# Kernel optimization log

Measured on AMD Instinct MI355X. Metric: run time of the kernel, lower is better.

## Reference

```python
import jax, jax.numpy as jnp
import numpy as np

N_NODES = 50000
N_EDGES = 1600000
DIM = 128
BN_EPS = 1e-5


def setup_inputs() -> dict:
    key = jax.random.key(0)
    k1, k2, k3 = jax.random.split(key, 3)
    x = jax.random.normal(k1, (N_NODES, DIM), dtype=jnp.float32)
    edge_index = jax.random.randint(k2, (2, N_EDGES), 0, N_NODES, dtype=jnp.int32)
    W = jax.random.normal(k3, (DIM, DIM), dtype=jnp.float32) / np.float32(np.sqrt(DIM))
    b = jnp.zeros((DIM,), dtype=jnp.float32)
    gamma = jnp.ones((DIM,), dtype=jnp.float32)
    beta = jnp.zeros((DIM,), dtype=jnp.float32)
    return {"x": x, "W": W, "b": b, "gamma": gamma, "beta": beta, "edge_index": edge_index}


def reference(x, W, b, gamma, beta, edge_index):
    """ResGCNBlock: relu(BN(GCNConv(x, edge_index))) + x (PyG GCNConv semantics)."""
    n = x.shape[0]
    # GCNConv: linear transform first
    h = x @ W  # [N, D]
    # add self-loops
    loop = jnp.arange(n, dtype=edge_index.dtype)
    src = jnp.concatenate([edge_index[0], loop])  # [E+N]
    dst = jnp.concatenate([edge_index[1], loop])
    # symmetric normalization: deg over targets (edge weight = 1)
    deg = jax.ops.segment_sum(jnp.ones_like(dst, dtype=h.dtype), dst, num_segments=n)
    dinv = jax.lax.rsqrt(jnp.maximum(deg, 1e-12))  # deg >= 1 due to self-loops
    norm = dinv[src] * dinv[dst]  # [E+N]
    # gather -> scale -> scatter-add
    agg = jax.ops.segment_sum(h[src] * norm[:, None], dst, num_segments=n) + b  # [N, D]
    # BatchNorm1d (training mode: batch stats over node dim, biased variance)
    mean = jnp.mean(agg, axis=0)
    var = jnp.mean(jnp.square(agg - mean), axis=0)
    y = gamma * (agg - mean) * jax.lax.rsqrt(var + BN_EPS) + beta
    return jax.nn.relu(y) + x
```

## Files before the change

### kernel.cpp

```cpp
#include <hip/hip_runtime.h>

#define DIM 128

__device__ __forceinline__ float bf_to_f(unsigned short v) {
    return __uint_as_float(((unsigned int)v) << 16);
}
__device__ __forceinline__ unsigned short f_to_bf(float f) {
    unsigned int u = __float_as_uint(f);
    u += 0x7FFFu + ((u >> 16) & 1u);
    return (unsigned short)(u >> 16);
}
__device__ __forceinline__ bool probe_bf16(const void* gamma) {
    return *reinterpret_cast<const unsigned int*>(gamma) != 0x3F800000u;
}

__global__ __launch_bounds__(256) void k_deg(const int* __restrict__ ei,
                                             int* __restrict__ deg, int E) {
    int t = blockIdx.x * 256 + threadIdx.x;
    if (t < E) atomicAdd(&deg[ei[E + t]], 1);
}
__global__ __launch_bounds__(256) void k_dinv(const int* __restrict__ deg,
                                              float* __restrict__ dinv, int N) {
    int t = blockIdx.x * 256 + threadIdx.x;
    if (t < N) dinv[t] = rsqrtf((float)deg[t] + 1.0f);
}

#define EPB 4096

__global__ __launch_bounds__(256) void k_cbhist(const int* __restrict__ ei,
                                                int* __restrict__ thist, int E) {
    __shared__ int hist[256];
    const int t = threadIdx.x;
    const int e0 = blockIdx.x * EPB;
    hist[t] = 0;
    __syncthreads();
    #pragma unroll
    for (int u = 0; u < 16; u++) {
        const int i = e0 + t + u * 256;
        if (i < E) atomicAdd(&hist[((unsigned int)ei[E + i]) >> 8], 1);
    }
    __syncthreads();
    if (hist[t] > 0) atomicAdd(&thist[t], hist[t]);
}

__global__ __launch_bounds__(256) void k_bscan2(const int* __restrict__ thist,
                                                int* __restrict__ bbase,
                                                int* __restrict__ ccur) {
    __shared__ int sh[256];
    const int t = threadIdx.x;
    const int v = thist[t];
    sh[t] = v;
    __syncthreads();
    for (int off = 1; off < 256; off <<= 1) {
        int u = (t >= off) ? sh[t - off] : 0;
        __syncthreads();
        sh[t] += u;
        __syncthreads();
    }
    bbase[t + 1] = sh[t];
    ccur[t] = sh[t] - v;
    if (t == 0) bbase[0] = 0;
}

__global__ __launch_bounds__(256) void k_partition(
    const int* __restrict__ ei, int* __restrict__ ccur,
    unsigned int* __restrict__ epart, int E)
{
    __shared__ int hist[256];
    __shared__ int scan_tmp[256];
    __shared__ int lbase[256];
    __shared__ int lcur[256];
    __shared__ int gbase[256];
    __shared__ unsigned int sorted[EPB];
    const int t = threadIdx.x;
    const int e0 = blockIdx.x * EPB;
    const int ecount = min(EPB, E - e0);
    hist[t] = 0; lcur[t] = 0;
    __syncthreads();

    unsigned int ent[16];
    #pragma unroll
    for (int u = 0; u < 16; u++) {
        const int i = e0 + t + u * 256;
        if (i < E) {
            const unsigned int src = (unsigned int)ei[i];
            const unsigned int dst = (unsigned int)ei[E + i];
            const unsigned int cb = dst >> 8;
            ent[u] = src | ((dst & 255u) << 16) | (cb << 24);
            atomicAdd(&hist[cb], 1);
        } else ent[u] = 0xFFFFFFFFu;
    }
    __syncthreads();
    scan_tmp[t] = hist[t];
    __syncthreads();
    for (int off = 1; off < 256; off <<= 1) {
        int v = (t >= off) ? scan_tmp[t - off] : 0;
        __syncthreads();
        scan_tmp[t] += v;
        __syncthreads();
    }
    lbase[t] = scan_tmp[t] - hist[t];
    __syncthreads();
    #pragma unroll
    for (int u = 0; u < 16; u++) {
        if (ent[u] != 0xFFFFFFFFu) {
            const int cb = (int)(ent[u] >> 24);
            const int pos = lbase[cb] + atomicAdd(&lcur[cb], 1);
            sorted[pos] = ent[u];
        }
    }
    if (hist[t] > 0) gbase[t] = atomicAdd(&ccur[t], hist[t]);
    __syncthreads();
    for (int s = t; s < ecount; s += 256) {
        const unsigned int e = sorted[s];
        const int cb = (int)(e >> 24);
        epart[gbase[cb] + (s - lbase[cb])] = e;
    }
}

__global__ __launch_bounds__(256) void k_fine2(
    const unsigned int* __restrict__ epart, const int* __restrict__ bbase,
    int* __restrict__ rowptr, float* __restrict__ dinv,
    int* __restrict__ esrc, int N)
{
    __shared__ int ldeg[256];
    __shared__ int sh[256];
    __shared__ int lex[256];
    __shared__ int lcur[256];
    const int cb = blockIdx.x;
    const int t = threadIdx.x;
    const int beg = bbase[cb];
    const int end = bbase[cb + 1];
    ldeg[t] = 0; lcur[t] = 0;
    __syncthreads();

    for (int i = beg + t; i < end; i += 256)
        atomicAdd(&ldeg[(epart[i] >> 16) & 255u], 1);
    __syncthreads();
    sh[t] = ldeg[t];
    __syncthreads();
    for (int off = 1; off < 256; off <<= 1) {
        int v = (t >= off) ? sh[t - off] : 0;
        __syncthreads();
        sh[t] += v;
        __syncthreads();
    }
    lex[t] = sh[t] - ldeg[t];
    __syncthreads();

    const int node = (cb << 8) + t;
    if (node < N) {
        rowptr[node] = beg + lex[t];
        dinv[node] = rsqrtf((float)ldeg[t] + 1.0f);
        if (node == N - 1) rowptr[N] = beg + lex[t] + ldeg[t];
    }

    for (int i = beg + t; i < end; i += 256) {
        const unsigned int e = epart[i];
        const int d = (int)((e >> 16) & 255u);
        const int pos = beg + lex[d] + atomicAdd(&lcur[d], 1);
        esrc[pos] = (int)(e & 0xFFFFu);
    }
}

__global__ __launch_bounds__(256, 4) void k_gemm(
    const void* __restrict__ xv, const void* __restrict__ Wv,
    const void* __restrict__ bv, const void* __restrict__ probe,
    const float* __restrict__ dinv, unsigned short* __restrict__ h,
    float* __restrict__ agg, int N, int wr_seed)
{
    const bool isbf = probe_bf16(probe);
    __shared__ __align__(16) unsigned short Wsb[DIM * 64];
    __shared__ __align__(16) float xs[64 * 132];
    const int t  = threadIdx.x;
    const int ch = blockIdx.x & 1;
    const int r0 = (blockIdx.x >> 1) * 64;

    if (isbf) {
        const unsigned short* W = (const unsigned short*)Wv;
        for (int s = 4 * t; s < DIM * 64; s += 1024) {
            const int k = s >> 6, c = s & 63;
            *reinterpret_cast<ushort4*>(Wsb + s) =
                *reinterpret_cast<const ushort4*>(W + k * DIM + ch * 64 + c);
        }
    } else {
        const float* W = (const float*)Wv;
        for (int s = 4 * t; s < DIM * 64; s += 1024) {
            const int k = s >> 6, c = s & 63;
            const float4 w = *reinterpret_cast<const float4*>(W + k * DIM + ch * 64 + c);
            ushort4 p;
            p.x = f_to_bf(w.x); p.y = f_to_bf(w.y);
            p.z = f_to_bf(w.z); p.w = f_to_bf(w.w);
            *reinterpret_cast<ushort4*>(Wsb + s) = p;
        }
    }
    for (int idx = 4 * t; idx < 64 * DIM; idx += 1024) {
        const int row = idx >> 7, k = idx & 127;
        const int r = r0 + row;
        float4 v = make_float4(0.f, 0.f, 0.f, 0.f);
        if (r < N) {
            if (isbf) {
                ushort4 u = *reinterpret_cast<const ushort4*>(
                    (const unsigned short*)xv + (size_t)r * DIM + k);
                v.x = bf_to_f(u.x); v.y = bf_to_f(u.y);
                v.z = bf_to_f(u.z); v.w = bf_to_f(u.w);
            } else {
                v = *reinterpret_cast<const float4*>((const float*)xv + (size_t)r * DIM + k);
            }
        }
        *reinterpret_cast<float4*>(xs + row * 132 + k) = v;
    }
    __syncthreads();

    const int c4 = t & 15;
    const int rg = t >> 4;
    float acc[4][4] = {{0,0,0,0},{0,0,0,0},{0,0,0,0},{0,0,0,0}};
    #pragma unroll 2
    for (int k = 0; k < DIM; k += 4) {
        const ushort4 wu0 = *reinterpret_cast<const ushort4*>(Wsb + (k + 0) * 64 + 4 * c4);
        const ushort4 wu1 = *reinterpret_cast<const ushort4*>(Wsb + (k + 1) * 64 + 4 * c4);
        const ushort4 wu2 = *reinterpret_cast<const ushort4*>(Wsb + (k + 2) * 64 + 4 * c4);
        const ushort4 wu3 = *reinterpret_cast<const ushort4*>(Wsb + (k + 3) * 64 + 4 * c4);
        float w[4][4];
        w[0][0] = bf_to_f(wu0.x); w[0][1] = bf_to_f(wu0.y);
        w[0][2] = bf_to_f(wu0.z); w[0][3] = bf_to_f(wu0.w);
        w[1][0] = bf_to_f(wu1.x); w[1][1] = bf_to_f(wu1.y);
        w[1][2] = bf_to_f(wu1.z); w[1][3] = bf_to_f(wu1.w);
        w[2][0] = bf_to_f(wu2.x); w[2][1] = bf_to_f(wu2.y);
        w[2][2] = bf_to_f(wu2.z); w[2][3] = bf_to_f(wu2.w);
        w[3][0] = bf_to_f(wu3.x); w[3][1] = bf_to_f(wu3.y);
        w[3][2] = bf_to_f(wu3.z); w[3][3] = bf_to_f(wu3.w);
        #pragma unroll
        for (int j = 0; j < 4; j++) {
            const float4 xk = *reinterpret_cast<const float4*>(&xs[(rg + 16 * j) * 132 + k]);
            #pragma unroll
            for (int cc = 0; cc < 4; cc++) {
                acc[j][cc] = fmaf(xk.x, w[0][cc], acc[j][cc]);
                acc[j][cc] = fmaf(xk.y, w[1][cc], acc[j][cc]);
                acc[j][cc] = fmaf(xk.z, w[2][cc], acc[j][cc]);
                acc[j][cc] = fmaf(xk.w, w[3][cc], acc[j][cc]);
            }
        }
    }
    const int gc = ch * 64 + 4 * c4;
    #pragma unroll
    for (int j = 0; j < 4; j++) {
        const int r = r0 + rg + 16 * j;
        if (r < N) {
            const float di = dinv[r];
            ushort4 hp;
            hp.x = f_to_bf(acc[j][0] * di); hp.y = f_to_bf(acc[j][1] * di);
            hp.z = f_to_bf(acc[j][2] * di); hp.w = f_to_bf(acc[j][3] * di);
            *reinterpret_cast<ushort4*>(h + (size_t)r * DIM + gc) = hp;
            if (wr_seed) {
                float4 bc;
                if (isbf) {
                    const unsigned short* bb = (const unsigned short*)bv;
                    bc.x = bf_to_f(bb[gc]); bc.y = bf_to_f(bb[gc + 1]);
                    bc.z = bf_to_f(bb[gc + 2]); bc.w = bf_to_f(bb[gc + 3]);
                } else {
                    bc = *reinterpret_cast<const float4*>((const float*)bv + gc);
                }
                const float di2 = di * di;
                float4 av;
                av.x = fmaf(acc[j][0], di2, bc.x);
                av.y = fmaf(acc[j][1], di2, bc.y);
                av.z = fmaf(acc[j][2], di2, bc.z);
                av.w = fmaf(acc[j][3], di2, bc.w);
                *reinterpret_cast<float4*>(agg + (size_t)r * DIM + gc) = av;
            }
        }
    }
}

__device__ __forceinline__ float2 load_h2(const unsigned short* __restrict__ h,
                                          int src, int lane) {
    const unsigned int u = *reinterpret_cast<const unsigned int*>(
        h + (size_t)src * DIM + 2 * lane);
    return make_float2(bf_to_f((unsigned short)(u & 0xFFFFu)),
                       bf_to_f((unsigned short)(u >> 16)));
}

__global__ __launch_bounds__(256) void k_agg(
    const int* __restrict__ rowptr, const int* __restrict__ esrc,
    const unsigned short* __restrict__ h, const float* __restrict__ dinv,
    const void* __restrict__ bv, const void* __restrict__ probe,
    float* __restrict__ agg, int N)
{
    const int lane = threadIdx.x & 63;
    const int node = __builtin_amdgcn_readfirstlane(
        (int)((blockIdx.x * 256 + threadIdx.x) >> 6));
    if (node >= N) return;

    const int beg = rowptr[node];
    const int end = rowptr[node + 1];
    const float didst = dinv[node];
    const unsigned int* __restrict__ hu = (const unsigned int*)h;

    float a0 = 0.f, a1 = 0.f;

    {
        const unsigned int v = hu[(size_t)node * 64 + lane];
        a0 += __uint_as_float(v << 16);
        a1 += __uint_as_float(v & 0xFFFF0000u);
    }

    const int lm = end - 1;
    for (int j = beg; j < end; j += 16) {
        const int myidx = esrc[min(j + (lane & 15), lm)];
        unsigned int uv[16];
        #pragma unroll
        for (int u = 0; u < 16; u++) {
            const int s = __builtin_amdgcn_readlane(myidx, u);
            uv[u] = hu[(size_t)s * 64 + lane];
        }
        #pragma unroll
        for (int u = 0; u < 16; u++) {
            const float sel = (j + u < end) ? 1.0f : 0.0f;
            a0 = fmaf(__uint_as_float(uv[u] << 16), sel, a0);
            a1 = fmaf(__uint_as_float(uv[u] & 0xFFFF0000u), sel, a1);
        }
    }

    const int gc = 2 * lane;
    float b0, b1;
    if (probe_bf16(probe)) {
        const unsigned int bb = *reinterpret_cast<const unsigned int*>(
            (const unsigned short*)bv + gc);
        b0 = bf_to_f((unsigned short)(bb & 0xFFFFu));
        b1 = bf_to_f((unsigned short)(bb >> 16));
    } else {
        const float2 bf = *reinterpret_cast<const float2*>((const float*)bv + gc);
        b0 = bf.x; b1 = bf.y;
    }
    float2 o;
    o.x = fmaf(a0, didst, b0);
    o.y = fmaf(a1, didst, b1);
    *reinterpret_cast<float2*>(agg + (size_t)node * DIM + gc) = o;
}

__global__ __launch_bounds__(256) void k_scatter(
    const int* __restrict__ ei, const unsigned short* __restrict__ h,
    const float* __restrict__ dinv, float* __restrict__ agg, int E)
{
    const int w = (blockIdx.x * 256 + threadIdx.x) >> 6;
    if (w >= E) return;
    const int lane = threadIdx.x & 63;
    const int src = ei[w];
    const int dst = ei[E + w];
    const float norm = dinv[dst];
    const float2 h2 = load_h2(h, src, lane);
    float* a = agg + (size_t)dst * DIM + 2 * lane;
    unsafeAtomicAdd(a + 0, h2.x * norm);
    unsafeAtomicAdd(a + 1, h2.y * norm);
}

__global__ __launch_bounds__(256) void k_stats(
    const float* __restrict__ agg, float* __restrict__ stats, int N, int rpb)
{
    __shared__ float ls[256];
    __shared__ float ls2[256];
    const int c = threadIdx.x & 127;
    const int half = threadIdx.x >> 7;
    const int r0 = blockIdx.x * rpb;
    const int r1 = min(r0 + rpb, N);
    float s = 0.f, s2 = 0.f;
    for (int r = r0 + half; r < r1; r += 2) {
        const float v = agg[(size_t)r * DIM + c];
        s += v;
        s2 = fmaf(v, v, s2);
    }
    ls[threadIdx.x] = s;
    ls2[threadIdx.x] = s2;
    __syncthreads();
    if (threadIdx.x < 128) {
        s  = ls[threadIdx.x]  + ls[threadIdx.x + 128];
        s2 = ls2[threadIdx.x] + ls2[threadIdx.x + 128];
        unsafeAtomicAdd(&stats[c], s);
        unsafeAtomicAdd(&stats[128 + c], s2);
    }
}

__global__ __launch_bounds__(256) void k_out(
    const float* __restrict__ agg, const void* __restrict__ xv,
    const void* __restrict__ gv, const void* __restrict__ bev,
    const float* __restrict__ stats, void* __restrict__ outv,
    float inv_n, int total4)
{
    __shared__ __align__(16) float ssc[128];
    __shared__ __align__(16) float ssh[128];
    const bool isbf = probe_bf16(gv);
    const int tt = threadIdx.x;
    if (tt < 128) {
        const float gamma = isbf ? bf_to_f(((const unsigned short*)gv)[tt])
                                 : ((const float*)gv)[tt];
        const float beta  = isbf ? bf_to_f(((const unsigned short*)bev)[tt])
                                 : ((const float*)bev)[tt];
        const float mean = stats[tt] * inv_n;
        const float var = fmaf(-mean, mean, stats[128 + tt] * inv_n);
        const float rs = rsqrtf(var + 1e-5f);
        const float scale = gamma * rs;
        ssc[tt] = scale;
        ssh[tt] = fmaf(-mean, scale, beta);
    }
    __syncthreads();
    const int t = blockIdx.x * 256 + tt;
    if (t >= total4) return;
    const int c4 = (t & 31) * 4;
    const float4 a = *reinterpret_cast<const float4*>(agg + (size_t)t * 4);
    const float4 sc = *reinterpret_cast<const float4*>(ssc + c4);
    const float4 sh = *reinterpret_cast<const float4*>(ssh + c4);
    float x0, x1, x2, x3;
    if (isbf) {
        const ushort4 u = *reinterpret_cast<const ushort4*>(
            (const unsigned short*)xv + (size_t)t * 4);
        x0 = bf_to_f(u.x); x1 = bf_to_f(u.y); x2 = bf_to_f(u.z); x3 = bf_to_f(u.w);
    } else {
        const float4 xf = *reinterpret_cast<const float4*>((const float*)xv + (size_t)t * 4);
        x0 = xf.x; x1 = xf.y; x2 = xf.z; x3 = xf.w;
    }
    const float y0 = fmaxf(fmaf(a.x, sc.x, sh.x), 0.f) + x0;
    const float y1 = fmaxf(fmaf(a.y, sc.y, sh.y), 0.f) + x1;
    const float y2 = fmaxf(fmaf(a.z, sc.z, sh.z), 0.f) + x2;
    const float y3 = fmaxf(fmaf(a.w, sc.w, sh.w), 0.f) + x3;
    if (isbf) {
        ushort4 o;
        o.x = f_to_bf(y0); o.y = f_to_bf(y1); o.z = f_to_bf(y2); o.w = f_to_bf(y3);
        *reinterpret_cast<ushort4*>((unsigned short*)outv + (size_t)t * 4) = o;
    } else {
        *reinterpret_cast<float4*>((float*)outv + (size_t)t * 4) =
            make_float4(y0, y1, y2, y3);
    }
}

extern "C" void kernel_launch(void* const* d_in, const int* in_sizes, int n_in,
                              void* d_out, int out_size, void* d_ws, size_t ws_size,
                              hipStream_t stream)
{
    const void* x     = d_in[0];
    const void* W     = d_in[1];
    const void* b     = d_in[2];
    const void* gamma = d_in[3];
    const void* beta  = d_in[4];
    const int*  ei    = (const int*)d_in[5];

    const int N = in_sizes[0] / DIM;
    const int E = in_sizes[5] / 2;
    const int nb = (N + 255) >> 8;
    const int nblk = (E + EPB - 1) / EPB;

    char* ws = (char*)d_ws;
    int*          deg    = (int*)(ws + 0);
    float*        stats  = (float*)(ws + 200704);
    int*          thist  = (int*)(ws + 201728);
    float*        dinv   = (float*)(ws + 202752);
    int*          rowptr = (int*)(ws + 403456);
    int*          ccur   = (int*)(ws + 603904);
    int*          bbase  = (int*)(ws + 604928);
    float*        agg    = (float*)(ws + 606976);
    unsigned int* epart  = (unsigned int*)(ws + 606976);
    int*          esrc   = (int*)(ws + 26206976);
    unsigned short* h    = (unsigned short*)d_out;
    const bool use_csr = (ws_size >= 32606976u) && (N <= 65536);

    hipMemsetAsync(ws, 0, 202752, stream);

    if (use_csr) {
        k_cbhist<<<nblk, 256, 0, stream>>>(ei, thist, E);
        k_bscan2<<<1, 256, 0, stream>>>(thist, bbase, ccur);
        k_partition<<<nblk, 256, 0, stream>>>(ei, ccur, epart, E);
        k_fine2<<<nb, 256, 0, stream>>>(epart, bbase, rowptr, dinv, esrc, N);
    } else {
        k_deg<<<(E + 255) / 256, 256, 0, stream>>>(ei, deg, E);
        k_dinv<<<(N + 255) / 256, 256, 0, stream>>>(deg, dinv, N);
    }

    const int nrb = (N + 63) / 64;
    k_gemm<<<nrb * 2, 256, 0, stream>>>(x, W, b, gamma, dinv, h, agg, N,
                                        use_csr ? 0 : 1);

    if (use_csr) {
        const int nblk_agg = (N * 64 + 255) / 256;
        k_agg<<<nblk_agg, 256, 0, stream>>>(rowptr, esrc, h, dinv, b, gamma,
                                            agg, N);
    } else {
        k_scatter<<<(E + 3) / 4, 256, 0, stream>>>(ei, h, dinv, agg, E);
    }

    const int rpb = (N + 255) / 256;
    k_stats<<<256, 256, 0, stream>>>(agg, stats, N, rpb);

    const int total4 = N * DIM / 4;
    k_out<<<(total4 + 255) / 256, 256, 0, stream>>>(
        agg, x, gamma, beta, stats, d_out, 1.0f / (float)N, total4);
}
```

Baseline: 264.9 us.

## Replace scalar FMA GEMM with bf16 MFMA using hi/lo split of x

```diff
diff --git a/kernel.cpp b/kernel.cpp
--- a/kernel.cpp
+++ b/kernel.cpp
@@ -163,111 +163,121 @@
     }
 }
 
-__global__ __launch_bounds__(256, 4) void k_gemm(
+typedef short bfrag8 __attribute__((ext_vector_type(8)));
+typedef float facc4 __attribute__((ext_vector_type(4)));
+
+__global__ __launch_bounds__(256) void k_gemm(
     const void* __restrict__ xv, const void* __restrict__ Wv,
     const void* __restrict__ bv, const void* __restrict__ probe,
     const float* __restrict__ dinv, unsigned short* __restrict__ h,
     float* __restrict__ agg, int N, int wr_seed)
 {
     const bool isbf = probe_bf16(probe);
-    __shared__ __align__(16) unsigned short Wsb[DIM * 64];
-    __shared__ __align__(16) float xs[64 * 132];
-    const int t  = threadIdx.x;
-    const int ch = blockIdx.x & 1;
-    const int r0 = (blockIdx.x >> 1) * 64;
-
-    if (isbf) {
-        const unsigned short* W = (const unsigned short*)Wv;
-        for (int s = 4 * t; s < DIM * 64; s += 1024) {
-            const int k = s >> 6, c = s & 63;
-            *reinterpret_cast<ushort4*>(Wsb + s) =
-                *reinterpret_cast<const ushort4*>(W + k * DIM + ch * 64 + c);
-        }
-    } else {
-        const float* W = (const float*)Wv;
-        for (int s = 4 * t; s < DIM * 64; s += 1024) {
-            const int k = s >> 6, c = s & 63;
-            const float4 w = *reinterpret_cast<const float4*>(W + k * DIM + ch * 64 + c);
-            ushort4 p;
-            p.x = f_to_bf(w.x); p.y = f_to_bf(w.y);
-            p.z = f_to_bf(w.z); p.w = f_to_bf(w.w);
-            *reinterpret_cast<ushort4*>(Wsb + s) = p;
-        }
-    }
-    for (int idx = 4 * t; idx < 64 * DIM; idx += 1024) {
-        const int row = idx >> 7, k = idx & 127;
+    __shared__ __align__(16) unsigned short xh[64 * 128];
+    __shared__ __align__(16) unsigned short xl[64 * 128];
+    __shared__ __align__(16) unsigned short wt[128 * 128];
+    const int t = threadIdx.x;
+    const int r0 = blockIdx.x * 64;
+
+    for (int s = t; s < 1024; s += 256) {
+        const int row = s >> 4;
+        const int kc8 = s & 15;
         const int r = r0 + row;
-        float4 v = make_float4(0.f, 0.f, 0.f, 0.f);
+        const int off = row * 128 + ((kc8 ^ (row & 7)) << 3);
+        unsigned short hi[8], lo[8];
         if (r < N) {
             if (isbf) {
-                ushort4 u = *reinterpret_cast<const ushort4*>(
-                    (const unsigned short*)xv + (size_t)r * DIM + k);
-                v.x = bf_to_f(u.x); v.y = bf_to_f(u.y);
-                v.z = bf_to_f(u.z); v.w = bf_to_f(u.w);
+                *reinterpret_cast<uint4*>(hi) = *reinterpret_cast<const uint4*>(
+                    (const unsigned short*)xv + (size_t)r * DIM + kc8 * 8);
+                #pragma unroll
+                for (int j = 0; j < 8; j++) lo[j] = 0;
             } else {
-                v = *reinterpret_cast<const float4*>((const float*)xv + (size_t)r * DIM + k);
+                const float* xp = (const float*)xv + (size_t)r * DIM + kc8 * 8;
+                const float4 v0 = *reinterpret_cast<const float4*>(xp);
+                const float4 v1 = *reinterpret_cast<const float4*>(xp + 4);
+                const float f[8] = {v0.x, v0.y, v0.z, v0.w, v1.x, v1.y, v1.z, v1.w};
+                #pragma unroll
+                for (int j = 0; j < 8; j++) {
+                    hi[j] = f_to_bf(f[j]);
+                    lo[j] = f_to_bf(f[j] - bf_to_f(hi[j]));
+                }
             }
-        }
-        *reinterpret_cast<float4*>(xs + row * 132 + k) = v;
-    }
-    __syncthreads();
-
-    const int c4 = t & 15;
-    const int rg = t >> 4;
-    float acc[4][4] = {{0,0,0,0},{0,0,0,0},{0,0,0,0},{0,0,0,0}};
-    #pragma unroll 2
-    for (int k = 0; k < DIM; k += 4) {
-        const ushort4 wu0 = *reinterpret_cast<const ushort4*>(Wsb + (k + 0) * 64 + 4 * c4);
-        const ushort4 wu1 = *reinterpret_cast<const ushort4*>(Wsb + (k + 1) * 64 + 4 * c4);
-        const ushort4 wu2 = *reinterpret_cast<const ushort4*>(Wsb + (k + 2) * 64 + 4 * c4);
-        const ushort4 wu3 = *reinterpret_cast<const ushort4*>(Wsb + (k + 3) * 64 + 4 * c4);
-        float w[4][4];
-        w[0][0] = bf_to_f(wu0.x); w[0][1] = bf_to_f(wu0.y);
-        w[0][2] = bf_to_f(wu0.z); w[0][3] = bf_to_f(wu0.w);
-        w[1][0] = bf_to_f(wu1.x); w[1][1] = bf_to_f(wu1.y);
-        w[1][2] = bf_to_f(wu1.z); w[1][3] = bf_to_f(wu1.w);
-        w[2][0] = bf_to_f(wu2.x); w[2][1] = bf_to_f(wu2.y);
-        w[2][2] = bf_to_f(wu2.z); w[2][3] = bf_to_f(wu2.w);
-        w[3][0] = bf_to_f(wu3.x); w[3][1] = bf_to_f(wu3.y);
-        w[3][2] = bf_to_f(wu3.z); w[3][3] = bf_to_f(wu3.w);
+        } else {
+            #pragma unroll
+            for (int j = 0; j < 8; j++) { hi[j] = 0; lo[j] = 0; }
+        }
+        *reinterpret_cast<uint4*>(&xh[off]) = *reinterpret_cast<const uint4*>(hi);
+        *reinterpret_cast<uint4*>(&xl[off]) = *reinterpret_cast<const uint4*>(lo);
+    }
+    for (int s = t; s < 2048; s += 256) {
+        const int col = s & 127;
+        const int kc8 = s >> 7;
+        unsigned short wv[8];
+        if (isbf) {
+            const unsigned short* Wp = (const unsigned short*)Wv;
+            #pragma unroll
+            for (int j = 0; j < 8; j++)
+                wv[j] = Wp[(size_t)(kc8 * 8 + j) * DIM + col];
+        } else {
+            const float* Wp = (const float*)Wv;
+            #pragma unroll
+            for (int j = 0; j < 8; j++)
+                wv[j] = f_to_bf(Wp[(size_t)(kc8 * 8 + j) * DIM + col]);
+        }
+        const int off = col * 128 + ((kc8 ^ (col & 7)) << 3);
+        *reinterpret_cast<uint4*>(&wt[off]) = *reinterpret_cast<const uint4*>(wv);
+    }
+    __syncthreads();
+
+    const int lane = t & 63;
+    const int w = t >> 6;
+    const int wrow = w * 16;
+    const int arow = wrow + (lane & 15);
+    const int kg = lane >> 4;
+
+    facc4 acc[8];
+    #pragma unroll
+    for (int ct = 0; ct < 8; ct++) acc[ct] = facc4{0.f, 0.f, 0.f, 0.f};
+
+    #pragma unroll
+    for (int kk = 0; kk < 4; kk++) {
+        const int kc8a = kk * 4 + kg;
+        const int aoff = arow * 128 + ((kc8a ^ (arow & 7)) << 3);
+        const bfrag8 ah = *reinterpret_cast<const bfrag8*>(&xh[aoff]);
+        const bfrag8 al = *reinterpret_cast<const bfrag8*>(&xl[aoff]);
+        #pragma unroll
+        for (int ct = 0; ct < 8; ct++) {
+            const int col = ct * 16 + (lane & 15);
+            const bfrag8 bw = *reinterpret_cast<const bfrag8*>(
+                &wt[col * 128 + ((kc8a ^ (col & 7)) << 3)]);
+            acc[ct] = __builtin_amdgcn_mfma_f32_16x16x32_bf16(al, bw, acc[ct], 0, 0, 0);
+            acc[ct] = __builtin_amdgcn_mfma_f32_16x16x32_bf16(ah, bw, acc[ct], 0, 0, 0);
+        }
+    }
+
+    const int colb = lane & 15;
+    const int m0 = (lane >> 4) * 4;
+    float di[4];
+    #pragma unroll
+    for (int j = 0; j < 4; j++) {
+        const int r = r0 + wrow + m0 + j;
+        di[j] = (r < N) ? dinv[r] : 0.f;
+    }
+    #pragma unroll
+    for (int ct = 0; ct < 8; ct++) {
+        const int col = ct * 16 + colb;
         #pragma unroll
         for (int j = 0; j < 4; j++) {
-            const float4 xk = *reinterpret_cast<const float4*>(&xs[(rg + 16 * j) * 132 + k]);
-            #pragma unroll
-            for (int cc = 0; cc < 4; cc++) {
-                acc[j][cc] = fmaf(xk.x, w[0][cc], acc[j][cc]);
-                acc[j][cc] = fmaf(xk.y, w[1][cc], acc[j][cc]);
-                acc[j][cc] = fmaf(xk.z, w[2][cc], acc[j][cc]);
-                acc[j][cc] = fmaf(xk.w, w[3][cc], acc[j][cc]);
-            }
-        }
-    }
-    const int gc = ch * 64 + 4 * c4;
-    #pragma unroll
-    for (int j = 0; j < 4; j++) {
-        const int r = r0 + rg + 16 * j;
-        if (r < N) {
-            const float di = dinv[r];
-            ushort4 hp;
-            hp.x = f_to_bf(acc[j][0] * di); hp.y = f_to_bf(acc[j][1] * di);
-            hp.z = f_to_bf(acc[j][2] * di); hp.w = f_to_bf(acc[j][3] * di);
-            *reinterpret_cast<ushort4*>(h + (size_t)r * DIM + gc) = hp;
-            if (wr_seed) {
-                float4 bc;
-                if (isbf) {
-                    const unsigned short* bb = (const unsigned short*)bv;
-                    bc.x = bf_to_f(bb[gc]); bc.y = bf_to_f(bb[gc + 1]);
-                    bc.z = bf_to_f(bb[gc + 2]); bc.w = bf_to_f(bb[gc + 3]);
-                } else {
-                    bc = *reinterpret_cast<const float4*>((const float*)bv + gc);
+            const int r = r0 + wrow + m0 + j;
+            if (r < N) {
+                h[(size_t)r * DIM + col] = f_to_bf(acc[ct][j] * di[j]);
+                if (wr_seed) {
+                    float bc;
+                    if (isbf) bc = bf_to_f(((const unsigned short*)bv)[col]);
+                    else      bc = ((const float*)bv)[col];
+                    agg[(size_t)r * DIM + col] =
+                        fmaf(acc[ct][j] * di[j], di[j], bc);
                 }
-                const float di2 = di * di;
-                float4 av;
-                av.x = fmaf(acc[j][0], di2, bc.x);
-                av.y = fmaf(acc[j][1], di2, bc.y);
-                av.z = fmaf(acc[j][2], di2, bc.z);
-                av.w = fmaf(acc[j][3], di2, bc.w);
-                *reinterpret_cast<float4*>(agg + (size_t)r * DIM + gc) = av;
             }
         }
     }
@@ -476,8 +486,8 @@
     }
 
     const int nrb = (N + 63) / 64;
-    k_gemm<<<nrb * 2, 256, 0, stream>>>(x, W, b, gamma, dinv, h, agg, N,
-                                        use_csr ? 0 : 1);
+    k_gemm<<<nrb, 256, 0, stream>>>(x, W, b, gamma, dinv, h, agg, N,
+                                    use_csr ? 0 : 1);
 
     if (use_csr) {
         const int nblk_agg = (N * 64 + 255) / 256;
```

Result: faster. 249.9 us (-5.7%).
